# Kernel tuning notes

Measured on AMD Instinct MI355X. Metric: run time of the kernel, lower is better.

Reference implementation:

```python
import jax, jax.numpy as jnp
import numpy as np

H = 16      # q heads
G = 4       # groups (n_rep)
THETA = 10000.0


def _rope(x, cos, sin):
    # x pairs adjacent elements (torch complex view of reshape(..., -1, 2))
    x0 = x[..., ::2]
    x1 = x[..., 1::2]
    r0 = x0 * cos - x1 * sin
    r1 = x0 * sin + x1 * cos
    return jnp.stack([r0, r1], axis=-1).reshape(x.shape)


def setup_inputs() -> dict:
    key = jax.random.key(0)
    ks = jax.random.split(key, 5)
    B, S, D = 2, 2048, 1024
    return {
        "x": jax.random.normal(ks[0], (B, S, D), jnp.float32),
        "Wq": jax.random.normal(ks[1], (D, D), jnp.float32) * 0.02,
        "Wk": jax.random.normal(ks[2], (D, D // G), jnp.float32) * 0.02,
        "Wv": jax.random.normal(ks[3], (D, D // G), jnp.float32) * 0.02,
        "Wo": jax.random.normal(ks[4], (D, D), jnp.float32) * 0.02,
    }


def reference(x, Wq, Wk, Wv, Wo):
    B, S, D = x.shape
    hd = D // H                     # head dim = 64
    Hkv = H // G                    # kv heads = 4

    q = x @ Wq                      # (B,S,D)
    k = x @ Wk                      # (B,S,D/G)
    v = x @ Wv                      # (B,S,D/G)

    # repeat_kv: (B,S,Hkv,hd) -> (B,S,H,hd)
    k = jnp.repeat(k.reshape(B, S, Hkv, hd), G, axis=2)
    v = jnp.repeat(v.reshape(B, S, Hkv, hd), G, axis=2)

    # RoPE angles: freqs precomputed over hidden_dim (as in source)
    inv = 1.0 / (THETA ** (jnp.arange(0, D, 2, dtype=jnp.float32) / D))  # (D/2,)
    ang = jnp.arange(S, dtype=jnp.float32)[:, None] * inv[None, :]       # (S,D/2)
    q = _rope(q, jnp.cos(ang)[None], jnp.sin(ang)[None])                 # (B,S,D)
    angk = ang[:, : hd // 2]                                             # (S,hd/2)
    k = _rope(k, jnp.cos(angk)[None, :, None, :], jnp.sin(angk)[None, :, None, :])

    q = q.reshape(B, S, H, hd).transpose(0, 2, 1, 3)   # (B,H,S,hd)
    k = k.transpose(0, 2, 1, 3)
    v = v.transpose(0, 2, 1, 3)

    # NOTE: scale uses sqrt(hidden_dim), faithful to source
    scores = jnp.einsum('bhqd,bhkd->bhqk', q, k) / jnp.sqrt(jnp.float32(D))
    p = jax.nn.softmax(scores, axis=-1)
    o = jnp.einsum('bhqk,bhkd->bhqd', p, v)
    o = o.transpose(0, 2, 1, 3).reshape(B, S, D)
    return o @ Wo
```

## Files before the change

kernel.cpp:

```cpp
#include <hip/hip_runtime.h>
#include <math.h>

#define BATCH 2
#define SEQ   2048
#define DMODEL 1024
#define KDIM  1024
#define NH    16
#define HDIM  64
#define GRP   4
#define NKV   4
#define NSPLIT 2

enum { M_PLAIN = 0, M_QKV = 1 };

#define LN_THETA 9.210340371976184f
#define QSCALE 0.04508422002778f

typedef short bf8_t __attribute__((ext_vector_type(8)));
typedef float f4_t __attribute__((ext_vector_type(4)));
typedef unsigned short us4_t __attribute__((ext_vector_type(4)));
typedef unsigned short us8_t __attribute__((ext_vector_type(8)));
typedef _Float16 h_t;
typedef _Float16 h4_t __attribute__((ext_vector_type(4)));

#define QB_OFF 0
#define KB_OFF 4194304
#define VB_OFF (4194304 + 1048576)

__device__ __forceinline__ unsigned short f2bf(float f) {
  unsigned int u = __float_as_uint(f);
  u += 0x7fffu + ((u >> 16) & 1u);
  return (unsigned short)(u >> 16);
}

__device__ __forceinline__ float fexp2(float x) {
#if __has_builtin(__builtin_amdgcn_exp2f)
  return __builtin_amdgcn_exp2f(x);
#else
  return exp2f(x);
#endif
}

__device__ __forceinline__ void gload_lds16(const void* g, void* l) {
  typedef __attribute__((address_space(1))) unsigned int gu32;
  typedef __attribute__((address_space(3))) unsigned int lu32;
  __builtin_amdgcn_global_load_lds((const gu32*)g, (lu32*)l, 16, 0, 0);
}

__global__ __launch_bounds__(256) void conv_x(const float* __restrict__ in,
                                              unsigned short* __restrict__ out) {
  const int i = blockIdx.x * 256 + threadIdx.x;
  float4 v = ((const float4*)in)[i];
  us4_t o = {f2bf(v.x), f2bf(v.y), f2bf(v.z), f2bf(v.w)};
  ((us4_t*)out)[i] = o;
}

__global__ __launch_bounds__(256) void convT_all(const float* __restrict__ W0,
                                                 const float* __restrict__ W1,
                                                 const float* __restrict__ W2,
                                                 const float* __restrict__ W3,
                                                 unsigned short* __restrict__ Wqkvt,
                                                 unsigned short* __restrict__ Wot) {
  const float* W; unsigned short* out; int N, rowoff;
  switch (blockIdx.z) {
    case 0: W = W0; out = Wqkvt; N = 1024; rowoff = 0;    break;
    case 1: W = W1; out = Wqkvt; N = 256;  rowoff = 1024; break;
    case 2: W = W2; out = Wqkvt; N = 256;  rowoff = 1280; break;
    default: W = W3; out = Wot;  N = 1024; rowoff = 0;    break;
  }
  const int n0 = blockIdx.x * 64;
  if (n0 >= N) return;
  __shared__ unsigned short T[64][72];
  const int t = threadIdx.x;
  const int k0 = blockIdx.y * 64;
  const int kr = t >> 4, n4 = (t & 15) * 4;
#pragma unroll
  for (int i = 0; i < 4; ++i) {
    const int k = kr + i * 16;
    float4 v = *(const float4*)&W[(size_t)(k0 + k) * N + n0 + n4];
    T[n4 + 0][k] = f2bf(v.x);
    T[n4 + 1][k] = f2bf(v.y);
    T[n4 + 2][k] = f2bf(v.z);
    T[n4 + 3][k] = f2bf(v.w);
  }
  __syncthreads();
#pragma unroll
  for (int i = 0; i < 2; ++i) {
    const int c = t + i * 256;
    const int n = c >> 3, kc = (c & 7) * 8;
    us8_t v = *(const us8_t*)&T[n][kc];
    *(us8_t*)&out[(size_t)(rowoff + n0 + n) * KDIM + k0 + kc] = v;
  }
}

template <int MODE>
__global__ __launch_bounds__(256, 3) void gemm_bf16(const unsigned short* __restrict__ A,
                                                    const unsigned short* __restrict__ Bt,
                                                    void* __restrict__ Cdst_, int N) {
  __shared__ __align__(16) unsigned short As[2 * 64 * 64];
  __shared__ __align__(16) unsigned short Bs[2 * 128 * 64];

  const int tid = threadIdx.x;
  const int lane = tid & 63, quad = lane >> 4, l16 = lane & 15;
  const int w = tid >> 6, wm = w >> 1, wn = w & 1;
  const int row0 = blockIdx.x * 64, col0 = blockIdx.y * 128;

  const int m0 = tid >> 2;
  const int kc0 = (tid & 3) ^ ((m0 >> 1) & 3);
  const unsigned short* Ag0 = A + (size_t)(row0 + m0) * KDIM + kc0 * 8;
  const unsigned short* Bg0 = Bt + (size_t)(col0 + m0) * KDIM + kc0 * 8;
  unsigned short* Al0 = &As[tid * 8];
  unsigned short* Bl0 = &Bs[tid * 8];

#define STAGE_GEMM(c, kk)                                                      \
  do {                                                                         \
    gload_lds16(Ag0 + (kk),      Al0 + (c) * 4096);                            \
    gload_lds16(Ag0 + (kk) + 32, Al0 + (c) * 4096 + 2048);                     \
    gload_lds16(Bg0 + (kk),                          Bl0 + (c) * 8192);        \
    gload_lds16(Bg0 + (size_t)64 * KDIM + (kk),      Bl0 + (c) * 8192 + 2048); \
    gload_lds16(Bg0 + (kk) + 32,                     Bl0 + (c) * 8192 + 4096); \
    gload_lds16(Bg0 + (size_t)64 * KDIM + (kk) + 32, Bl0 + (c) * 8192 + 6144); \
  } while (0)

  int aoff[2][2], boff[4][2];
#pragma unroll
  for (int mi = 0; mi < 2; ++mi) {
    const int am = wm * 32 + mi * 16 + l16;
    const int sw = quad ^ ((am >> 1) & 3);
#pragma unroll
    for (int kh = 0; kh < 2; ++kh)
      aoff[mi][kh] = kh * 2048 + (((am << 2) | sw) << 3);
  }
#pragma unroll
  for (int ni = 0; ni < 4; ++ni) {
    const int bn = wn * 64 + ni * 16 + l16;
    const int sw = quad ^ ((bn >> 1) & 3);
#pragma unroll
    for (int kh = 0; kh < 2; ++kh)
      boff[ni][kh] = kh * 4096 + (((bn << 2) | sw) << 3);
  }

  f4_t acc[2][4];
#pragma unroll
  for (int mi = 0; mi < 2; ++mi)
#pragma unroll
    for (int ni = 0; ni < 4; ++ni) acc[mi][ni] = (f4_t){0.f, 0.f, 0.f, 0.f};

  STAGE_GEMM(0, 0);
  __syncthreads();
  int cur = 0;
  for (int kb = 0; kb < KDIM; kb += 64) {
    if (kb + 64 < KDIM) STAGE_GEMM(cur ^ 1, kb + 64);

    const unsigned short* Asc = As + cur * 4096;
    const unsigned short* Bsc = Bs + cur * 8192;
    bf8_t af[2][2], bfr[4][2];
#pragma unroll
    for (int mi = 0; mi < 2; ++mi)
#pragma unroll
      for (int kh = 0; kh < 2; ++kh) af[mi][kh] = *(const bf8_t*)&Asc[aoff[mi][kh]];
#pragma unroll
    for (int ni = 0; ni < 4; ++ni)
#pragma unroll
      for (int kh = 0; kh < 2; ++kh) bfr[ni][kh] = *(const bf8_t*)&Bsc[boff[ni][kh]];
#pragma unroll
    for (int kh = 0; kh < 2; ++kh)
#pragma unroll
      for (int mi = 0; mi < 2; ++mi)
#pragma unroll
        for (int ni = 0; ni < 4; ++ni)
          acc[mi][ni] = __builtin_amdgcn_mfma_f32_16x16x32_bf16(af[mi][kh], bfr[ni][kh], acc[mi][ni], 0, 0, 0);

    __syncthreads();
    cur ^= 1;
  }
#undef STAGE_GEMM

  if constexpr (MODE == M_PLAIN) {
    float* out = (float*)Cdst_;
#pragma unroll
    for (int mi = 0; mi < 2; ++mi) {
      const int rowb = row0 + wm * 32 + mi * 16 + quad * 4;
#pragma unroll
      for (int ni = 0; ni < 4; ++ni) {
        const int n = col0 + wn * 64 + ni * 16 + l16;
#pragma unroll
        for (int r = 0; r < 4; ++r)
          out[(size_t)(rowb + r) * N + n] = acc[mi][ni][r];
      }
    }
  } else {
    unsigned short* Qb = (unsigned short*)Cdst_;
    unsigned short* Kb = Qb + (KB_OFF - QB_OFF);
    unsigned short* Vb = Qb + (VB_OFF - QB_OFF);
#pragma unroll
    for (int ni = 0; ni < 4; ++ni) {
      const int nb = col0 + wn * 64 + ni * 16;
      const int n = nb + l16;
      if (nb < 1024) {
        const float inv = expf(-(float)(2 * (n >> 1)) * (LN_THETA / (float)DMODEL));
        const float sgn = (n & 1) ? 1.f : -1.f;
        const int h = n >> 6, d = n & 63;
#pragma unroll
        for (int mi = 0; mi < 2; ++mi) {
          const int rowb = row0 + wm * 32 + mi * 16 + quad * 4;
#pragma unroll
          for (int r = 0; r < 4; ++r) {
            const int row = rowb + r;
            const int bb = row >> 11, s = row & (SEQ - 1);
            const float v = acc[mi][ni][r];
            const float p = __shfl_xor(v, 1);
            float sn, cs;
            sincosf((float)s * inv, &sn, &cs);
            const float res = (v * cs + sgn * p * sn) * QSCALE;
            Qb[((size_t)(bb * NH + h) * SEQ + s) * HDIM + d] = f2bf(res);
          }
        }
      } else if (nb < 1280) {
        const int nk = n - 1024;
        const int hkv = nk >> 6, d = nk & 63;
        const float inv = expf(-(float)(2 * (d >> 1)) * (LN_THETA / (float)DMODEL));
        const float sgn = (nk & 1) ? 1.f : -1.f;
#pragma unroll
        for (int mi = 0; mi < 2; ++mi) {
          const int rowb = row0 + wm * 32 + mi * 16 + quad * 4;
#pragma unroll
          for (int r = 0; r < 4; ++r) {
            const int row = rowb + r;
            const int bb = row >> 11, s = row & (SEQ - 1);
            const float v = acc[mi][ni][r];
            const float p = __shfl_xor(v, 1);
            float sn, cs;
            sincosf((float)s * inv, &sn, &cs);
            const float res = v * cs + sgn * p * sn;
            Kb[((size_t)(bb * NKV + hkv) * SEQ + s) * HDIM + d] = f2bf(res);
          }
        }
      } else {
        const int nv = n - 1280;
        const int hkv = nv >> 6, d = nv & 63;
#pragma unroll
        for (int mi = 0; mi < 2; ++mi) {
          const int s0 = row0 + wm * 32 + mi * 16 + quad * 4;
          const int bb = s0 >> 11, sl = s0 & (SEQ - 1);
          const int st = sl & 63;
          const int ps = (sl & ~63) | (st & 0x20) | ((st & 0x0C) << 1) | ((st & 0x10) >> 2);
          us4_t stv = {f2bf(acc[mi][ni][0]), f2bf(acc[mi][ni][1]),
                       f2bf(acc[mi][ni][2]), f2bf(acc[mi][ni][3])};
          *(us4_t*)&Vb[((size_t)(bb * NKV + hkv) * HDIM + d) * SEQ + ps] = stv;
        }
      }
    }
  }
}

__global__ __launch_bounds__(256, 4) void attn_fwd(const unsigned short* __restrict__ Q,
                                                   const unsigned short* __restrict__ K,
                                                   const unsigned short* __restrict__ V,
                                                   h_t* __restrict__ Opart,
                                                   float* __restrict__ Lpart) {
  __shared__ __align__(16) unsigned short Kt[2 * 4096];
  __shared__ __align__(16) unsigned short Vt[2 * 4096];

  const int b = blockIdx.x >> 4;
  const int h = blockIdx.x & (NH - 1);
  const int hkv = h >> 2;
  const int q0 = blockIdx.y * 128;
  const int sp = blockIdx.z;
  const int tid = threadIdx.x;
  const int w = tid >> 6;
  const int lane = tid & 63;
  const int quad = lane >> 4;
  const int l16 = lane & 15;

  const unsigned short* Qg = Q + ((size_t)(b * NH + h) * SEQ + q0 + w * 32) * HDIM;
  const unsigned short* Kg = K + (size_t)(b * NKV + hkv) * SEQ * HDIM;
  const unsigned short* Vg = V + (size_t)(b * NKV + hkv) * HDIM * SEQ;

  bf8_t qb[2][2];
#pragma unroll
  for (int g = 0; g < 2; ++g)
#pragma unroll
    for (int half = 0; half < 2; ++half)
      qb[g][half] = *(const bf8_t*)(Qg + (size_t)(g * 16 + l16) * HDIM + half * 32 + quad * 8);

  f4_t accO[2][4];
#pragma unroll
  for (int g = 0; g < 2; ++g)
#pragma unroll
    for (int d = 0; d < 4; ++d) accO[g][d] = (f4_t){0.f, 0.f, 0.f, 0.f};
  float accLs[2] = {0.f, 0.f};

  const int sw8 = (quad ^ ((l16 >> 1) & 3)) << 3;

  const int skey = tid >> 2;
  const int gc = ((tid & 3) ^ ((tid >> 3) & 3)) << 3;
  const unsigned short* KgA = Kg + (size_t)skey * HDIM + gc;
  const unsigned short* VgA = Vg + (size_t)skey * SEQ + gc;

#define STAGE_ATTN(c, kk)                                                          \
  do {                                                                             \
    gload_lds16(KgA + (size_t)(kk) * HDIM,      &Kt[(c) * 4096 + tid * 8]);        \
    gload_lds16(KgA + (size_t)(kk) * HDIM + 32, &Kt[(c) * 4096 + tid * 8 + 2048]); \
    gload_lds16(VgA + (kk),      &Vt[(c) * 4096 + tid * 8]);                       \
    gload_lds16(VgA + (kk) + 32, &Vt[(c) * 4096 + tid * 8 + 2048]);                \
  } while (0)

  const int kbeg = sp * (SEQ / NSPLIT);
  const int kend = kbeg + SEQ / NSPLIT;

  STAGE_ATTN(0, kbeg);
  __syncthreads();
  int cur = 0;
  for (int k0 = kbeg; k0 < kend; k0 += 64) {
    if (k0 + 64 < kend) STAGE_ATTN(cur ^ 1, k0 + 64);

    const unsigned short* Ktc = Kt + cur * 4096;
    const unsigned short* Vtc = Vt + cur * 4096;

    union { bf8_t bf; unsigned int dw[4]; } pa[2][2];
#pragma unroll
    for (int cb = 0; cb < 4; ++cb) {
      const int koff = (cb * 16 + l16) * 32 + sw8;
      bf8_t kf0 = *(const bf8_t*)&Ktc[koff];
      bf8_t kf1 = *(const bf8_t*)&Ktc[koff + 2048];
#pragma unroll
      for (int g = 0; g < 2; ++g) {
        f4_t s = (f4_t){0.f, 0.f, 0.f, 0.f};
        s = __builtin_amdgcn_mfma_f32_16x16x32_bf16(kf0, qb[g][0], s, 0, 0, 0);
        s = __builtin_amdgcn_mfma_f32_16x16x32_bf16(kf1, qb[g][1], s, 0, 0, 0);
        const float p0 = fexp2(s[0]), p1 = fexp2(s[1]);
        const float p2 = fexp2(s[2]), p3 = fexp2(s[3]);
        accLs[g] += (p0 + p1) + (p2 + p3);
        unsigned int w0, w1;
        asm("v_cvt_pk_bf16_f32 %0, %1, %2" : "=v"(w0) : "v"(p0), "v"(p1));
        asm("v_cvt_pk_bf16_f32 %0, %1, %2" : "=v"(w1) : "v"(p2), "v"(p3));
        pa[g][cb >> 1].dw[(cb & 1) * 2 + 0] = w0;
        pa[g][cb >> 1].dw[(cb & 1) * 2 + 1] = w1;
      }
    }

#pragma unroll
    for (int db = 0; db < 4; ++db) {
      const int voff = (db * 16 + l16) * 32 + sw8;
      bf8_t vf0 = *(const bf8_t*)&Vtc[voff];
      bf8_t vf1 = *(const bf8_t*)&Vtc[voff + 2048];
#pragma unroll
      for (int g = 0; g < 2; ++g) {
        accO[g][db] = __builtin_amdgcn_mfma_f32_16x16x32_bf16(pa[g][0].bf, vf0, accO[g][db], 0, 0, 0);
        accO[g][db] = __builtin_amdgcn_mfma_f32_16x16x32_bf16(pa[g][1].bf, vf1, accO[g][db], 0, 0, 0);
      }
    }

    __syncthreads();
    cur ^= 1;
  }
#undef STAGE_ATTN

#pragma unroll
  for (int g = 0; g < 2; ++g) {
    accLs[g] += __shfl_xor(accLs[g], 16);
    accLs[g] += __shfl_xor(accLs[g], 32);
  }

  h_t* Osp = Opart + (size_t)sp * BATCH * SEQ * NH * HDIM;
  float* Lsp = Lpart + (size_t)sp * BATCH * SEQ * NH;
#pragma unroll
  for (int g = 0; g < 2; ++g)
#pragma unroll
    for (int r = 0; r < 4; ++r) {
      const int q = q0 + w * 32 + g * 16 + quad * 4 + r;
      const size_t rowi = ((size_t)b * SEQ + q) * NH + h;
      h_t* op = Osp + rowi * HDIM;
#pragma unroll
      for (int db = 0; db < 4; ++db)
        op[db * 16 + l16] = (h_t)accO[g][db][r];
    }
  if (quad == 0) {
#pragma unroll
    for (int g = 0; g < 2; ++g) {
      const int q = q0 + w * 32 + g * 16 + l16;
      Lsp[((size_t)b * SEQ + q) * NH + h] = accLs[g];
    }
  }
}

__global__ __launch_bounds__(256) void attn_merge(const h_t* __restrict__ Opart,
                                                  const float* __restrict__ Lpart,
                                                  unsigned short* __restrict__ Ow) {
  const int idx = blockIdx.x * 256 + threadIdx.x;
  const int g = idx >> 4, j = (idx & 15) * 4;
  const size_t nq = (size_t)BATCH * SEQ * NH;
  float L = 0.f;
  float4 acc = make_float4(0.f, 0.f, 0.f, 0.f);
#pragma unroll
  for (int u = 0; u < NSPLIT; ++u) {
    L += Lpart[u * nq + g];
    h4_t o = *(const h4_t*)&Opart[((size_t)u * nq + g) * HDIM + j];
    acc.x += (float)o[0]; acc.y += (float)o[1];
    acc.z += (float)o[2]; acc.w += (float)o[3];
  }
  const float il = 1.0f / L;
  us4_t o = {f2bf(acc.x * il), f2bf(acc.y * il), f2bf(acc.z * il), f2bf(acc.w * il)};
  *(us4_t*)&Ow[(size_t)g * HDIM + j] = o;
}

extern "C" void kernel_launch(void* const* d_in, const int* in_sizes, int n_in,
                              void* d_out, int out_size, void* d_ws, size_t ws_size,
                              hipStream_t stream) {
  (void)in_sizes; (void)n_in; (void)out_size; (void)ws_size;
  const float* x  = (const float*)d_in[0];
  const float* Wq = (const float*)d_in[1];
  const float* Wk = (const float*)d_in[2];
  const float* Wv = (const float*)d_in[3];
  const float* Wo = (const float*)d_in[4];
  float* out = (float*)d_out;

  unsigned short* Qb    = (unsigned short*)d_ws;
  unsigned short* Kb    = Qb + 4194304;
  unsigned short* Vb    = Kb + 1048576;
  unsigned short* xb    = Vb + 1048576;
  unsigned short* Owb   = xb + 4194304;
  unsigned short* Wqkvt = Owb + 4194304;
  unsigned short* Wot   = Wqkvt + 1572864;
  h_t* Opart = (h_t*)(Wot + 1048576);
  float* Lpart = (float*)(Opart + (size_t)NSPLIT * 4194304);

  dim3 blk(256);
  conv_x<<<dim3(4096), blk, 0, stream>>>(x, xb);
  convT_all<<<dim3(16, 16, 4), blk, 0, stream>>>(Wq, Wk, Wv, Wo, Wqkvt, Wot);

  gemm_bf16<M_QKV><<<dim3(64, 12), blk, 0, stream>>>(xb, Wqkvt, Qb, 1536);
  attn_fwd<<<dim3(BATCH * NH, SEQ / 128, NSPLIT), blk, 0, stream>>>(Qb, Kb, Vb, Opart, Lpart);
  attn_merge<<<dim3(4096), blk, 0, stream>>>(Opart, Lpart, Owb);
  gemm_bf16<M_PLAIN><<<dim3(64, 8), blk, 0, stream>>>(Owb, Wot, out, DMODEL);
}
```

Measured before the change: 171.3 us.

## Pre-pack GEMM operands into MFMA fragment layout and drop LDS staging

The producers (x conversion, weight transpose, attention merge) now write bf16 operands directly in a 16x32 MFMA-fragment-tiled layout. The GEMM becomes an LDS-free kernel where each wave loads its fragments straight from global memory with register double buffering and computes a 64x64 tile. This removes shared-memory staging, swizzling and barriers. The cost is reuse: operands are shared only through L2 rather than LDS, so global and L2 traffic goes up.

```diff
diff --git a/kernel.cpp b/kernel.cpp
--- a/kernel.cpp
+++ b/kernel.cpp
@@ -27,6 +27,8 @@
 #define KB_OFF 4194304
 #define VB_OFF (4194304 + 1048576)
 
+#define KT32 (KDIM / 32)
+
 __device__ __forceinline__ unsigned short f2bf(float f) {
   unsigned int u = __float_as_uint(f);
   u += 0x7fffu + ((u >> 16) & 1u);
@@ -49,10 +51,17 @@
 
 __global__ __launch_bounds__(256) void conv_x(const float* __restrict__ in,
                                               unsigned short* __restrict__ out) {
-  const int i = blockIdx.x * 256 + threadIdx.x;
-  float4 v = ((const float4*)in)[i];
-  us4_t o = {f2bf(v.x), f2bf(v.y), f2bf(v.z), f2bf(v.w)};
-  ((us4_t*)out)[i] = o;
+  const int t = blockIdx.x * 256 + threadIdx.x;
+  const int row = t >> 7;
+  const int k = (t & 127) * 8;
+  const float* src = in + (size_t)row * DMODEL + k;
+  float4 v0 = *(const float4*)src;
+  float4 v1 = *(const float4*)(src + 4);
+  const int lanep = (row & 15) + ((k >> 3) & 3) * 16;
+  const size_t dst = (((size_t)(row >> 4) * KT32 + (k >> 5)) * 64 + lanep) * 8;
+  us8_t o = {f2bf(v0.x), f2bf(v0.y), f2bf(v0.z), f2bf(v0.w),
+             f2bf(v1.x), f2bf(v1.y), f2bf(v1.z), f2bf(v1.w)};
+  *(us8_t*)&out[dst] = o;
 }
 
 __global__ __launch_bounds__(256) void convT_all(const float* __restrict__ W0,
@@ -89,101 +98,69 @@
     const int c = t + i * 256;
     const int n = c >> 3, kc = (c & 7) * 8;
     us8_t v = *(const us8_t*)&T[n][kc];
-    *(us8_t*)&out[(size_t)(rowoff + n0 + n) * KDIM + k0 + kc] = v;
+    const int gn = rowoff + n0 + n;
+    const int gk = k0 + kc;
+    const int lanep = (gn & 15) + ((gk >> 3) & 3) * 16;
+    const size_t dst = (((size_t)(gn >> 4) * KT32 + (gk >> 5)) * 64 + lanep) * 8;
+    *(us8_t*)&out[dst] = v;
   }
 }
 
 template <int MODE>
-__global__ __launch_bounds__(256, 3) void gemm_bf16(const unsigned short* __restrict__ A,
-                                                    const unsigned short* __restrict__ Bt,
-                                                    void* __restrict__ Cdst_, int N) {
-  __shared__ __align__(16) unsigned short As[2 * 64 * 64];
-  __shared__ __align__(16) unsigned short Bs[2 * 128 * 64];
-
+__global__ __launch_bounds__(128) void gemm_frag(const unsigned short* __restrict__ A,
+                                                 const unsigned short* __restrict__ Bt,
+                                                 void* __restrict__ Cdst_, int N) {
   const int tid = threadIdx.x;
-  const int lane = tid & 63, quad = lane >> 4, l16 = lane & 15;
-  const int w = tid >> 6, wm = w >> 1, wn = w & 1;
-  const int row0 = blockIdx.x * 64, col0 = blockIdx.y * 128;
-
-  const int m0 = tid >> 2;
-  const int kc0 = (tid & 3) ^ ((m0 >> 1) & 3);
-  const unsigned short* Ag0 = A + (size_t)(row0 + m0) * KDIM + kc0 * 8;
-  const unsigned short* Bg0 = Bt + (size_t)(col0 + m0) * KDIM + kc0 * 8;
-  unsigned short* Al0 = &As[tid * 8];
-  unsigned short* Bl0 = &Bs[tid * 8];
-
-#define STAGE_GEMM(c, kk)                                                      \
-  do {                                                                         \
-    gload_lds16(Ag0 + (kk),      Al0 + (c) * 4096);                            \
-    gload_lds16(Ag0 + (kk) + 32, Al0 + (c) * 4096 + 2048);                     \
-    gload_lds16(Bg0 + (kk),                          Bl0 + (c) * 8192);        \
-    gload_lds16(Bg0 + (size_t)64 * KDIM + (kk),      Bl0 + (c) * 8192 + 2048); \
-    gload_lds16(Bg0 + (kk) + 32,                     Bl0 + (c) * 8192 + 4096); \
-    gload_lds16(Bg0 + (size_t)64 * KDIM + (kk) + 32, Bl0 + (c) * 8192 + 6144); \
+  const int lane = tid & 63;
+  const int wv = tid >> 6;
+  const int quad = lane >> 4, l16 = lane & 15;
+  const int rt0 = blockIdx.y * 4;
+  const int ct0 = (blockIdx.x * 2 + wv) * 4;
+
+  const unsigned short* Ag = A + ((size_t)rt0 * KT32) * 512 + lane * 8;
+  const unsigned short* Bg = Bt + ((size_t)ct0 * KT32) * 512 + lane * 8;
+
+  f4_t acc[4][4];
+#pragma unroll
+  for (int mi = 0; mi < 4; ++mi)
+#pragma unroll
+    for (int ni = 0; ni < 4; ++ni) acc[mi][ni] = (f4_t){0.f, 0.f, 0.f, 0.f};
+
+  bf8_t aX[4], bX[4], aY[4], bY[4];
+
+#define LDF(AS, BS, kt)                                                  \
+  do {                                                                   \
+    _Pragma("unroll") for (int i = 0; i < 4; ++i)                        \
+        AS[i] = *(const bf8_t*)(Ag + ((size_t)i * KT32 + (kt)) * 512);   \
+    _Pragma("unroll") for (int i = 0; i < 4; ++i)                        \
+        BS[i] = *(const bf8_t*)(Bg + ((size_t)i * KT32 + (kt)) * 512);   \
   } while (0)
-
-  int aoff[2][2], boff[4][2];
-#pragma unroll
-  for (int mi = 0; mi < 2; ++mi) {
-    const int am = wm * 32 + mi * 16 + l16;
-    const int sw = quad ^ ((am >> 1) & 3);
-#pragma unroll
-    for (int kh = 0; kh < 2; ++kh)
-      aoff[mi][kh] = kh * 2048 + (((am << 2) | sw) << 3);
-  }
-#pragma unroll
-  for (int ni = 0; ni < 4; ++ni) {
-    const int bn = wn * 64 + ni * 16 + l16;
-    const int sw = quad ^ ((bn >> 1) & 3);
-#pragma unroll
-    for (int kh = 0; kh < 2; ++kh)
-      boff[ni][kh] = kh * 4096 + (((bn << 2) | sw) << 3);
-  }
-
-  f4_t acc[2][4];
-#pragma unroll
-  for (int mi = 0; mi < 2; ++mi)
-#pragma unroll
-    for (int ni = 0; ni < 4; ++ni) acc[mi][ni] = (f4_t){0.f, 0.f, 0.f, 0.f};
-
-  STAGE_GEMM(0, 0);
-  __syncthreads();
-  int cur = 0;
-  for (int kb = 0; kb < KDIM; kb += 64) {
-    if (kb + 64 < KDIM) STAGE_GEMM(cur ^ 1, kb + 64);
-
-    const unsigned short* Asc = As + cur * 4096;
-    const unsigned short* Bsc = Bs + cur * 8192;
-    bf8_t af[2][2], bfr[4][2];
-#pragma unroll
-    for (int mi = 0; mi < 2; ++mi)
-#pragma unroll
-      for (int kh = 0; kh < 2; ++kh) af[mi][kh] = *(const bf8_t*)&Asc[aoff[mi][kh]];
-#pragma unroll
-    for (int ni = 0; ni < 4; ++ni)
-#pragma unroll
-      for (int kh = 0; kh < 2; ++kh) bfr[ni][kh] = *(const bf8_t*)&Bsc[boff[ni][kh]];
-#pragma unroll
-    for (int kh = 0; kh < 2; ++kh)
-#pragma unroll
-      for (int mi = 0; mi < 2; ++mi)
-#pragma unroll
-        for (int ni = 0; ni < 4; ++ni)
-          acc[mi][ni] = __builtin_amdgcn_mfma_f32_16x16x32_bf16(af[mi][kh], bfr[ni][kh], acc[mi][ni], 0, 0, 0);
-
-    __syncthreads();
-    cur ^= 1;
-  }
-#undef STAGE_GEMM
+#define FMAS(AS, BS)                                                     \
+  do {                                                                   \
+    _Pragma("unroll") for (int mi = 0; mi < 4; ++mi)                     \
+        _Pragma("unroll") for (int ni = 0; ni < 4; ++ni)                 \
+            acc[mi][ni] = __builtin_amdgcn_mfma_f32_16x16x32_bf16(       \
+                AS[mi], BS[ni], acc[mi][ni], 0, 0, 0);                   \
+  } while (0)
+
+  LDF(aX, bX, 0);
+  for (int kt = 0; kt < KT32; kt += 2) {
+    LDF(aY, bY, kt + 1);
+    FMAS(aX, bX);
+    if (kt + 2 < KT32) LDF(aX, bX, kt + 2);
+    FMAS(aY, bY);
+  }
+#undef LDF
+#undef FMAS
 
   if constexpr (MODE == M_PLAIN) {
     float* out = (float*)Cdst_;
 #pragma unroll
-    for (int mi = 0; mi < 2; ++mi) {
-      const int rowb = row0 + wm * 32 + mi * 16 + quad * 4;
+    for (int mi = 0; mi < 4; ++mi) {
+      const int rowb = (rt0 + mi) * 16 + quad * 4;
 #pragma unroll
       for (int ni = 0; ni < 4; ++ni) {
-        const int n = col0 + wn * 64 + ni * 16 + l16;
+        const int n = (ct0 + ni) * 16 + l16;
 #pragma unroll
         for (int r = 0; r < 4; ++r)
           out[(size_t)(rowb + r) * N + n] = acc[mi][ni][r];
@@ -195,15 +172,15 @@
     unsigned short* Vb = Qb + (VB_OFF - QB_OFF);
 #pragma unroll
     for (int ni = 0; ni < 4; ++ni) {
-      const int nb = col0 + wn * 64 + ni * 16;
+      const int nb = (ct0 + ni) * 16;
       const int n = nb + l16;
       if (nb < 1024) {
         const float inv = expf(-(float)(2 * (n >> 1)) * (LN_THETA / (float)DMODEL));
         const float sgn = (n & 1) ? 1.f : -1.f;
         const int h = n >> 6, d = n & 63;
 #pragma unroll
-        for (int mi = 0; mi < 2; ++mi) {
-          const int rowb = row0 + wm * 32 + mi * 16 + quad * 4;
+        for (int mi = 0; mi < 4; ++mi) {
+          const int rowb = (rt0 + mi) * 16 + quad * 4;
 #pragma unroll
           for (int r = 0; r < 4; ++r) {
             const int row = rowb + r;
@@ -222,8 +199,8 @@
         const float inv = expf(-(float)(2 * (d >> 1)) * (LN_THETA / (float)DMODEL));
         const float sgn = (nk & 1) ? 1.f : -1.f;
 #pragma unroll
-        for (int mi = 0; mi < 2; ++mi) {
-          const int rowb = row0 + wm * 32 + mi * 16 + quad * 4;
+        for (int mi = 0; mi < 4; ++mi) {
+          const int rowb = (rt0 + mi) * 16 + quad * 4;
 #pragma unroll
           for (int r = 0; r < 4; ++r) {
             const int row = rowb + r;
@@ -240,8 +217,8 @@
         const int nv = n - 1280;
         const int hkv = nv >> 6, d = nv & 63;
 #pragma unroll
-        for (int mi = 0; mi < 2; ++mi) {
-          const int s0 = row0 + wm * 32 + mi * 16 + quad * 4;
+        for (int mi = 0; mi < 4; ++mi) {
+          const int s0 = (rt0 + mi) * 16 + quad * 4;
           const int bb = s0 >> 11, sl = s0 & (SEQ - 1);
           const int st = sl & 63;
           const int ps = (sl & ~63) | (st & 0x20) | ((st & 0x0C) << 1) | ((st & 0x10) >> 2);
@@ -402,7 +379,11 @@
   }
   const float il = 1.0f / L;
   us4_t o = {f2bf(acc.x * il), f2bf(acc.y * il), f2bf(acc.z * il), f2bf(acc.w * il)};
-  *(us4_t*)&Ow[(size_t)g * HDIM + j] = o;
+  const int r = g >> 4;
+  const int c = (g & 15) * HDIM + j;
+  const int lanep = (r & 15) + ((c >> 3) & 3) * 16;
+  const size_t dst = (((size_t)(r >> 4) * KT32 + (c >> 5)) * 64 + lanep) * 8 + (c & 7);
+  *(us4_t*)&Ow[dst] = o;
 }
 
 extern "C" void kernel_launch(void* const* d_in, const int* in_sizes, int n_in,
@@ -427,11 +408,11 @@
   float* Lpart = (float*)(Opart + (size_t)NSPLIT * 4194304);
 
   dim3 blk(256);
-  conv_x<<<dim3(4096), blk, 0, stream>>>(x, xb);
+  conv_x<<<dim3(2048), blk, 0, stream>>>(x, xb);
   convT_all<<<dim3(16, 16, 4), blk, 0, stream>>>(Wq, Wk, Wv, Wo, Wqkvt, Wot);
 
-  gemm_bf16<M_QKV><<<dim3(64, 12), blk, 0, stream>>>(xb, Wqkvt, Qb, 1536);
+  gemm_frag<M_QKV><<<dim3(12, 64), dim3(128), 0, stream>>>(xb, Wqkvt, Qb, 1536);
   attn_fwd<<<dim3(BATCH * NH, SEQ / 128, NSPLIT), blk, 0, stream>>>(Qb, Kb, Vb, Opart, Lpart);
   attn_merge<<<dim3(4096), blk, 0, stream>>>(Opart, Lpart, Owb);
-  gemm_bf16<M_PLAIN><<<dim3(64, 8), blk, 0, stream>>>(Owb, Wot, out, DMODEL);
-}
+  gemm_frag<M_PLAIN><<<dim3(8, 64), dim3(128), 0, stream>>>(Owb, Wot, out, DMODEL);
+}
```

New measurement: 202.0 us. 1.18x slower.

## Replace double-buffered GEMM pipeline with single-buffered 128-wide K tiles

Applied to the files above, without the earlier changes.

The bf16 GEMM's main loop no longer double-buffers 64-wide K slices with prefetch of the next stage. It now loads a single 128-wide K tile into LDS, synchronizes, and computes, so there are half as many iterations and barriers per block. In exchange it loses the overlap between global-to-LDS loads and MFMA compute, so loads are fully exposed unless occupancy hides them.

```diff
diff --git a/kernel.cpp b/kernel.cpp
--- a/kernel.cpp
+++ b/kernel.cpp
@@ -97,8 +97,8 @@
 __global__ __launch_bounds__(256, 3) void gemm_bf16(const unsigned short* __restrict__ A,
                                                     const unsigned short* __restrict__ Bt,
                                                     void* __restrict__ Cdst_, int N) {
-  __shared__ __align__(16) unsigned short As[2 * 64 * 64];
-  __shared__ __align__(16) unsigned short Bs[2 * 128 * 64];
+  __shared__ __align__(16) unsigned short As[4 * 2048];
+  __shared__ __align__(16) unsigned short Bs[4 * 4096];
 
   const int tid = threadIdx.x;
   const int lane = tid & 63, quad = lane >> 4, l16 = lane & 15;
@@ -112,23 +112,13 @@
   unsigned short* Al0 = &As[tid * 8];
   unsigned short* Bl0 = &Bs[tid * 8];
 
-#define STAGE_GEMM(c, kk)                                                      \
-  do {                                                                         \
-    gload_lds16(Ag0 + (kk),      Al0 + (c) * 4096);                            \
-    gload_lds16(Ag0 + (kk) + 32, Al0 + (c) * 4096 + 2048);                     \
-    gload_lds16(Bg0 + (kk),                          Bl0 + (c) * 8192);        \
-    gload_lds16(Bg0 + (size_t)64 * KDIM + (kk),      Bl0 + (c) * 8192 + 2048); \
-    gload_lds16(Bg0 + (kk) + 32,                     Bl0 + (c) * 8192 + 4096); \
-    gload_lds16(Bg0 + (size_t)64 * KDIM + (kk) + 32, Bl0 + (c) * 8192 + 6144); \
-  } while (0)
-
-  int aoff[2][2], boff[4][2];
+  int aoff[2][4], boff[4][4];
 #pragma unroll
   for (int mi = 0; mi < 2; ++mi) {
     const int am = wm * 32 + mi * 16 + l16;
     const int sw = quad ^ ((am >> 1) & 3);
 #pragma unroll
-    for (int kh = 0; kh < 2; ++kh)
+    for (int kh = 0; kh < 4; ++kh)
       aoff[mi][kh] = kh * 2048 + (((am << 2) | sw) << 3);
   }
 #pragma unroll
@@ -136,7 +126,7 @@
     const int bn = wn * 64 + ni * 16 + l16;
     const int sw = quad ^ ((bn >> 1) & 3);
 #pragma unroll
-    for (int kh = 0; kh < 2; ++kh)
+    for (int kh = 0; kh < 4; ++kh)
       boff[ni][kh] = kh * 4096 + (((bn << 2) | sw) << 3);
   }
 
@@ -146,35 +136,30 @@
 #pragma unroll
     for (int ni = 0; ni < 4; ++ni) acc[mi][ni] = (f4_t){0.f, 0.f, 0.f, 0.f};
 
-  STAGE_GEMM(0, 0);
-  __syncthreads();
-  int cur = 0;
-  for (int kb = 0; kb < KDIM; kb += 64) {
-    if (kb + 64 < KDIM) STAGE_GEMM(cur ^ 1, kb + 64);
-
-    const unsigned short* Asc = As + cur * 4096;
-    const unsigned short* Bsc = Bs + cur * 8192;
-    bf8_t af[2][2], bfr[4][2];
-#pragma unroll
-    for (int mi = 0; mi < 2; ++mi)
-#pragma unroll
-      for (int kh = 0; kh < 2; ++kh) af[mi][kh] = *(const bf8_t*)&Asc[aoff[mi][kh]];
-#pragma unroll
-    for (int ni = 0; ni < 4; ++ni)
-#pragma unroll
-      for (int kh = 0; kh < 2; ++kh) bfr[ni][kh] = *(const bf8_t*)&Bsc[boff[ni][kh]];
-#pragma unroll
-    for (int kh = 0; kh < 2; ++kh)
+  for (int kb = 0; kb < KDIM; kb += 128) {
+    __syncthreads();
+#pragma unroll
+    for (int kh = 0; kh < 4; ++kh) {
+      gload_lds16(Ag0 + kb + kh * 32,                     Al0 + kh * 2048);
+      gload_lds16(Bg0 + kb + kh * 32,                     Bl0 + kh * 4096);
+      gload_lds16(Bg0 + (size_t)64 * KDIM + kb + kh * 32, Bl0 + kh * 4096 + 2048);
+    }
+    __syncthreads();
+
+#pragma unroll
+    for (int kh = 0; kh < 4; ++kh) {
+      bf8_t af[2], bfr[4];
+#pragma unroll
+      for (int mi = 0; mi < 2; ++mi) af[mi] = *(const bf8_t*)&As[aoff[mi][kh]];
+#pragma unroll
+      for (int ni = 0; ni < 4; ++ni) bfr[ni] = *(const bf8_t*)&Bs[boff[ni][kh]];
 #pragma unroll
       for (int mi = 0; mi < 2; ++mi)
 #pragma unroll
         for (int ni = 0; ni < 4; ++ni)
-          acc[mi][ni] = __builtin_amdgcn_mfma_f32_16x16x32_bf16(af[mi][kh], bfr[ni][kh], acc[mi][ni], 0, 0, 0);
-
-    __syncthreads();
-    cur ^= 1;
-  }
-#undef STAGE_GEMM
+          acc[mi][ni] = __builtin_amdgcn_mfma_f32_16x16x32_bf16(af[mi], bfr[ni], acc[mi][ni], 0, 0, 0);
+    }
+  }
 
   if constexpr (MODE == M_PLAIN) {
     float* out = (float*)Cdst_;
```

New measurement: 165.7 us. 3.3% less time.
